# Optimization experiments

Hardware: AMD Instinct MI355X
Metric: run time of the kernel (lower is better)

The kernel has to match this reference:

```python
import jax, jax.numpy as jnp
import numpy as np

N_HEADS = 16


def setup_inputs() -> dict:
    key = jax.random.key(0)
    ks = jax.random.split(key, 5)
    B, S, D = 2, 2048, 1024
    H = N_HEADS
    return {
        "queries": jax.random.normal(ks[0], (B, S, D), dtype=jnp.float32),
        "keys": jax.random.normal(ks[1], (B, S, D), dtype=jnp.float32),
        "values": jax.random.normal(ks[2], (B, S, D), dtype=jnp.float32),
        "bias": jax.random.normal(ks[3], (1, H, S, S), dtype=jnp.float32) * 0.02,
        "w_out": jax.random.normal(ks[4], (D, D), dtype=jnp.float32) * (1.0 / np.sqrt(D)),
    }


def _split_heads(x, n_heads):
    B, S, D = x.shape
    return x.reshape(B, S, n_heads, D // n_heads).transpose(0, 2, 1, 3)  # [B,H,S,hd]


def reference(queries, keys, values, bias, w_out):
    H = N_HEADS
    q = _split_heads(queries, H)
    k = _split_heads(keys, H)
    v = _split_heads(values, H)
    hd = k.shape[-1]
    # NOTE: original adds bias to raw logits, THEN scales by 1/sqrt(dk)
    logits = jnp.einsum("bhqd,bhkd->bhqk", q, k) + bias
    weights = jax.nn.softmax(logits * (1.0 / np.sqrt(hd)), axis=-1)
    attn = jnp.einsum("bhqk,bhkd->bhqd", weights, v)  # [B,H,Sq,hd]
    B, _, Sq, _ = attn.shape
    combined = attn.transpose(0, 2, 1, 3).reshape(B, Sq, H * hd)
    return combined @ w_out
```

## Files before the change

kernel.cpp:

```cpp
#include <hip/hip_runtime.h>

typedef float  f32x4  __attribute__((ext_vector_type(4)));
typedef short  bf16x8 __attribute__((ext_vector_type(8)));
typedef short  s16x4  __attribute__((ext_vector_type(4)));
typedef unsigned int u32x4 __attribute__((ext_vector_type(4)));

#define MFMA_BF16 __builtin_amdgcn_mfma_f32_16x16x32_bf16

__device__ __forceinline__ short f2bf(float f) {
  union { float f; unsigned u; } x; x.f = f;
  unsigned r = x.u + 0x7FFFu + ((x.u >> 16) & 1u);
  return (short)(r >> 16);
}

constexpr int S = 2048, D = 1024, H = 16, HD = 64;
constexpr int NT = S / 64;
constexpr float SCALE = 0.125f;
constexpr float L2E = 1.44269504f;
constexpr float SL = SCALE * L2E;

#define GLDS16(g, l) __builtin_amdgcn_global_load_lds( \
    (const __attribute__((address_space(1))) unsigned*)(g), \
    (__attribute__((address_space(3))) unsigned*)(l), 16, 0, 0)

__global__ __launch_bounds__(256)
void kv_prep(const float* __restrict__ Kg, const float* __restrict__ Vg,
             short* __restrict__ Kb, short* __restrict__ Vb) {
  const int tile = blockIdx.x, h = blockIdx.y, b = blockIdx.z;
  const int t = threadIdx.x, lane = t & 63, w = t >> 6;
  const int lg = lane >> 4, lm = lane & 15;
  __shared__ short kt[64 * 68], vt[64 * 68];
  const float* kp = Kg + ((size_t)(b * S + tile * 64)) * D + h * HD;
  const float* vp = Vg + ((size_t)(b * S + tile * 64)) * D + h * HD;
  #pragma unroll
  for (int i = 0; i < 4; ++i) {
    int idx = i * 256 + t, r = idx >> 4, c4 = (idx & 15) * 4;
    float4 k4 = *(const float4*)(kp + (size_t)r * D + c4);
    s16x4 ks; ks[0]=f2bf(k4.x); ks[1]=f2bf(k4.y); ks[2]=f2bf(k4.z); ks[3]=f2bf(k4.w);
    *(s16x4*)&kt[r * 68 + c4] = ks;
    float4 v4 = *(const float4*)(vp + (size_t)r * D + c4);
    s16x4 vs; vs[0]=f2bf(v4.x); vs[1]=f2bf(v4.y); vs[2]=f2bf(v4.z); vs[3]=f2bf(v4.w);
    *(s16x4*)&vt[r * 68 + c4] = vs;
  }
  __syncthreads();
  const size_t obase = ((size_t)((b * H + h) * NT + tile)) * 4096;
  #pragma unroll
  for (int j = 0; j < 2; ++j) {
    int f = w + j * 4, kk = f >> 2, mf = f & 3;
    int row = mf * 16 + lm, col = kk * 32 + lg * 4;
    s16x4 c0 = *(const s16x4*)&kt[row * 68 + col];
    s16x4 c1 = *(const s16x4*)&kt[row * 68 + col + 16];
    bf16x8 a;
    a[0]=c0[0]; a[1]=c0[1]; a[2]=c0[2]; a[3]=c0[3];
    a[4]=c1[0]; a[5]=c1[1]; a[6]=c1[2]; a[7]=c1[3];
    *(bf16x8*)&Kb[obase + (size_t)(f * 64 + lane) * 8] = a;
  }
  #pragma unroll
  for (int j = 0; j < 2; ++j) {
    int f = w + j * 4, kk = f >> 2, of = f & 3;
    int col = of * 16 + lm;
    bf16x8 a;
    #pragma unroll
    for (int half = 0; half < 2; ++half)
      #pragma unroll
      for (int e = 0; e < 4; ++e)
        a[half * 4 + e] = vt[(kk * 32 + lg * 4 + half * 16 + e) * 68 + col];
    *(bf16x8*)&Vb[obase + (size_t)(f * 64 + lane) * 8] = a;
  }
}

__device__ __forceinline__ void attn_tile(const short* kb, const short* vb,
                                          const f32x4* br, const bf16x8* qf,
                                          int lane, float& M, float& L, f32x4* o) {
  const f32x4 zero4 = {0.f, 0.f, 0.f, 0.f};
  f32x4 sacc[4];
  #pragma unroll
  for (int i = 0; i < 4; ++i) sacc[i] = zero4;
  #pragma unroll
  for (int kk = 0; kk < 2; ++kk)
    #pragma unroll
    for (int mf = 0; mf < 4; ++mf) {
      bf16x8 a = *(const bf16x8*)&kb[(kk * 4 + mf) * 512 + lane * 8];
      sacc[mf] = MFMA_BF16(a, qf[kk], sacc[mf], 0, 0, 0);
    }
  float p[4][4];
  float tmax = -__builtin_inff();
  #pragma unroll
  for (int mf = 0; mf < 4; ++mf)
    #pragma unroll
    for (int j = 0; j < 4; ++j) {
      float tv = (sacc[mf][j] + br[mf][j]) * SL;
      p[mf][j] = tv;
      tmax = fmaxf(tmax, tv);
    }
  tmax = fmaxf(tmax, __shfl_xor(tmax, 16, 64));
  tmax = fmaxf(tmax, __shfl_xor(tmax, 32, 64));
  const float Mn = fmaxf(M, tmax);
  const float alpha = exp2f(M - Mn);
  float psum = 0.f;
  #pragma unroll
  for (int mf = 0; mf < 4; ++mf)
    #pragma unroll
    for (int j = 0; j < 4; ++j) {
      float e = exp2f(p[mf][j] - Mn);
      p[mf][j] = e;
      psum += e;
    }
  psum += __shfl_xor(psum, 16, 64);
  psum += __shfl_xor(psum, 32, 64);
  L = L * alpha + psum;
  M = Mn;
  #pragma unroll
  for (int of = 0; of < 4; ++of) {
    o[of][0] *= alpha; o[of][1] *= alpha; o[of][2] *= alpha; o[of][3] *= alpha;
  }
  bf16x8 pb[2];
  #pragma unroll
  for (int kk = 0; kk < 2; ++kk)
    #pragma unroll
    for (int j = 0; j < 8; ++j)
      pb[kk][j] = f2bf(p[kk * 2 + (j >> 2)][j & 3]);
  #pragma unroll
  for (int kk = 0; kk < 2; ++kk)
    #pragma unroll
    for (int of = 0; of < 4; ++of) {
      bf16x8 a = *(const bf16x8*)&vb[(kk * 4 + of) * 512 + lane * 8];
      o[of] = MFMA_BF16(a, pb[kk], o[of], 0, 0, 0);
    }
}

__global__ __launch_bounds__(256, 4)
void attn_fused(const float* __restrict__ Qg, const float* __restrict__ Bg,
                const short* __restrict__ Kb, const short* __restrict__ Vb,
                short* __restrict__ comb) {
  __shared__ __attribute__((aligned(16))) short smem[16384];
  const int bid = blockIdx.x;
  const int rr = bid >> 4, x = bid & 15;
  const int pairidx = rr * 8 + (x & 7);
  const int b = x >> 3;
  const int h = pairidx >> 5, qt = pairidx & 31;
  const int q0 = qt * 64;
  const int t = threadIdx.x, lane = t & 63, w = t >> 6;
  const int lg = lane >> 4, lm = lane & 15;

  bf16x8 qf[2];
  {
    const float* qp = Qg + ((size_t)(b * S + q0 + w * 16 + lm)) * D + h * HD;
    #pragma unroll
    for (int kk = 0; kk < 2; ++kk)
      #pragma unroll
      for (int j = 0; j < 8; ++j)
        qf[kk][j] = f2bf(qp[kk * 32 + (j >> 2) * 16 + lg * 4 + (j & 3)]);
  }

  const short* Kt = Kb + ((size_t)(b * H + h) * NT) * 4096;
  const short* Vt = Vb + ((size_t)(b * H + h) * NT) * 4096;
  const float* bp = Bg + ((size_t)(h * S + q0 + w * 16 + lm)) * S + lg * 4;

  const f32x4 zero4 = {0.f, 0.f, 0.f, 0.f};
  f32x4 o[4];
  #pragma unroll
  for (int i = 0; i < 4; ++i) o[i] = zero4;
  float M = -__builtin_inff(), L = 0.f;

#define STAGE(tile, kdst, vdst)                                        \
  {                                                                    \
    const short* kg_ = Kt + (size_t)(tile) * 4096;                     \
    const short* vg_ = Vt + (size_t)(tile) * 4096;                     \
    _Pragma("unroll")                                                  \
    for (int r_ = 0; r_ < 2; ++r_) {                                   \
      GLDS16(kg_ + (size_t)((r_ * 4 + w) * 64 + lane) * 8,             \
             (kdst) + (r_ * 4 + w) * 512);                             \
      GLDS16(vg_ + (size_t)((r_ * 4 + w) * 64 + lane) * 8,             \
             (vdst) + (r_ * 4 + w) * 512);                             \
    }                                                                  \
  }

#define BLOAD(dst, tile)                                               \
  {                                                                    \
    const float* bq_ = bp + (tile) * 64;                               \
    dst[0] = *(const f32x4*)(bq_);                                     \
    dst[1] = *(const f32x4*)(bq_ + 16);                                \
    dst[2] = *(const f32x4*)(bq_ + 32);                                \
    dst[3] = *(const f32x4*)(bq_ + 48);                                \
  }

  f32x4 biasA[4], biasB[4];
  STAGE(0, smem, smem + 8192);
  BLOAD(biasA, 0);
  __syncthreads();

  for (int tt = 0; tt < NT; tt += 2) {
    STAGE(tt + 1, smem + 4096, smem + 12288);
    BLOAD(biasB, tt + 1);
    attn_tile(smem, smem + 8192, biasA, qf, lane, M, L, o);
    __syncthreads();
    if (tt + 2 < NT) {
      STAGE(tt + 2, smem, smem + 8192);
      BLOAD(biasA, tt + 2);
    }
    attn_tile(smem + 4096, smem + 12288, biasB, qf, lane, M, L, o);
    __syncthreads();
  }

  const float invL = 1.f / L;
  short* out_lds = smem;
  #pragma unroll
  for (int of = 0; of < 4; ++of)
    #pragma unroll
    for (int j = 0; j < 4; ++j)
      out_lds[(w * 16 + lm) * 72 + of * 16 + lg * 4 + j] = f2bf(o[of][j] * invL);
  __syncthreads();
  #pragma unroll
  for (int it = 0; it < 2; ++it) {
    int idx = it * 256 + t;
    int r = idx >> 3, seg = idx & 7;
    u32x4 u = *(const u32x4*)&out_lds[r * 72 + seg * 8];
    *(u32x4*)&comb[((size_t)(b * S + q0 + r)) * D + h * HD + seg * 8] = u;
  }
#undef STAGE
#undef BLOAD
}

__global__ __launch_bounds__(256)
void wt_kernel(const float* __restrict__ W, short* __restrict__ Wt) {
  __shared__ __attribute__((aligned(16))) short tile[64 * 72];
  const int n0 = blockIdx.x * 64, k0 = blockIdx.y * 64;
  const int t = threadIdx.x;
  #pragma unroll
  for (int i = 0; i < 4; ++i) {
    int idx = i * 256 + t;
    int r  = idx >> 4, c4 = (idx & 15) * 4;
    float4 wv = *(const float4*)(W + (size_t)(k0 + r) * D + n0 + c4);
    tile[(c4 + 0) * 72 + r] = f2bf(wv.x);
    tile[(c4 + 1) * 72 + r] = f2bf(wv.y);
    tile[(c4 + 2) * 72 + r] = f2bf(wv.z);
    tile[(c4 + 3) * 72 + r] = f2bf(wv.w);
  }
  __syncthreads();
  #pragma unroll
  for (int it = 0; it < 2; ++it) {
    int idx = it * 256 + t;
    int r = idx >> 3, seg = idx & 7;
    u32x4 u = *(const u32x4*)&tile[r * 72 + seg * 8];
    *(u32x4*)&Wt[(size_t)(n0 + r) * D + k0 + seg * 8] = u;
  }
}

__global__ __launch_bounds__(256, 2)
void proj_gemm(const short* __restrict__ A, const short* __restrict__ Bt,
               float* __restrict__ C) {
  constexpr int AST = 80;
  __shared__ __attribute__((aligned(16))) short a_lds[128 * AST];
  __shared__ __attribute__((aligned(16))) short b_lds[128 * AST];
  const int m0 = blockIdx.x * 128, n0 = blockIdx.y * 128;
  const int t = threadIdx.x, lane = t & 63, w = t >> 6;
  const int lg = lane >> 4, lm = lane & 15;
  const int wm = w >> 1, wn = w & 1;

  const f32x4 zero4 = {0.f, 0.f, 0.f, 0.f};
  f32x4 acc[4][4];
  #pragma unroll
  for (int i = 0; i < 4; ++i)
    #pragma unroll
    for (int j = 0; j < 4; ++j) acc[i][j] = zero4;

  for (int kt = 0; kt < D; kt += 64) {
    __syncthreads();
    #pragma unroll
    for (int i = 0; i < 4; ++i) {
      int idx = i * 256 + t;
      int r = idx >> 3, seg = idx & 7;
      u32x4 av = *(const u32x4*)&A [(size_t)(m0 + r) * D + kt + seg * 8];
      *(u32x4*)&a_lds[r * AST + seg * 8] = av;
      u32x4 bv = *(const u32x4*)&Bt[(size_t)(n0 + r) * D + kt + seg * 8];
      *(u32x4*)&b_lds[r * AST + seg * 8] = bv;
    }
    __syncthreads();
    #pragma unroll
    for (int kk = 0; kk < 2; ++kk) {
      bf16x8 af[4], bfr[4];
      #pragma unroll
      for (int mf = 0; mf < 4; ++mf) {
        const short* ar = &a_lds[(wm * 64 + mf * 16 + lm) * AST + kk * 32 + lg * 4];
        s16x4 c0 = *(const s16x4*)(ar);
        s16x4 c1 = *(const s16x4*)(ar + 16);
        af[mf][0]=c0[0]; af[mf][1]=c0[1]; af[mf][2]=c0[2]; af[mf][3]=c0[3];
        af[mf][4]=c1[0]; af[mf][5]=c1[1]; af[mf][6]=c1[2]; af[mf][7]=c1[3];
      }
      #pragma unroll
      for (int nf = 0; nf < 4; ++nf) {
        const short* br = &b_lds[(wn * 64 + nf * 16 + lm) * AST + kk * 32 + lg * 4];
        s16x4 c0 = *(const s16x4*)(br);
        s16x4 c1 = *(const s16x4*)(br + 16);
        bfr[nf][0]=c0[0]; bfr[nf][1]=c0[1]; bfr[nf][2]=c0[2]; bfr[nf][3]=c0[3];
        bfr[nf][4]=c1[0]; bfr[nf][5]=c1[1]; bfr[nf][6]=c1[2]; bfr[nf][7]=c1[3];
      }
      #pragma unroll
      for (int mf = 0; mf < 4; ++mf)
        #pragma unroll
        for (int nf = 0; nf < 4; ++nf)
          acc[mf][nf] = MFMA_BF16(af[mf], bfr[nf], acc[mf][nf], 0, 0, 0);
    }
  }
  #pragma unroll
  for (int mf = 0; mf < 4; ++mf)
    #pragma unroll
    for (int j = 0; j < 4; ++j)
      #pragma unroll
      for (int nf = 0; nf < 4; ++nf)
        C[(size_t)(m0 + wm * 64 + mf * 16 + lg * 4 + j) * D +
          n0 + wn * 64 + nf * 16 + lm] = acc[mf][nf][j];
}

extern "C" void kernel_launch(void* const* d_in, const int* in_sizes, int n_in,
                              void* d_out, int out_size, void* d_ws, size_t ws_size,
                              hipStream_t stream) {
  const float* Qg = (const float*)d_in[0];
  const float* Kg = (const float*)d_in[1];
  const float* Vg = (const float*)d_in[2];
  const float* Bg = (const float*)d_in[3];
  const float* Wg = (const float*)d_in[4];
  float* out = (float*)d_out;

  short* comb = (short*)d_ws;
  short* Wt   = comb + (size_t)(2 * S) * D;
  short* Kb   = Wt   + (size_t)D * D;
  short* Vb   = Kb   + (size_t)2 * H * NT * 4096;

  kv_prep<<<dim3(NT, H, 2), 256, 0, stream>>>(Kg, Vg, Kb, Vb);
  wt_kernel<<<dim3(D / 64, D / 64), 256, 0, stream>>>(Wg, Wt);
  attn_fused<<<dim3(1024), 256, 0, stream>>>(Qg, Bg, Kb, Vb, comb);
  proj_gemm<<<dim3((2 * S) / 128, D / 128), 256, 0, stream>>>(comb, Wt, out);
}
```

Baseline: 179.1 us.

## Pipeline projection GEMM with async LDS loads, swizzle, and finer barriers

```diff
diff --git a/kernel.cpp b/kernel.cpp
--- a/kernel.cpp
+++ b/kernel.cpp
@@ -8,9 +8,8 @@
 #define MFMA_BF16 __builtin_amdgcn_mfma_f32_16x16x32_bf16
 
 __device__ __forceinline__ short f2bf(float f) {
-  union { float f; unsigned u; } x; x.f = f;
-  unsigned r = x.u + 0x7FFFu + ((x.u >> 16) & 1u);
-  return (short)(r >> 16);
+  __bf16 h = (__bf16)f;
+  return __builtin_bit_cast(short, h);
 }
 
 constexpr int S = 2048, D = 1024, H = 16, HD = 64;
@@ -22,6 +21,9 @@
 #define GLDS16(g, l) __builtin_amdgcn_global_load_lds( \
     (const __attribute__((address_space(1))) unsigned*)(g), \
     (__attribute__((address_space(3))) unsigned*)(l), 16, 0, 0)
+
+#define WAITV(n) asm volatile("s_waitcnt vmcnt(" #n ")" ::: "memory")
+#define SBAR()   __builtin_amdgcn_s_barrier()
 
 __global__ __launch_bounds__(256)
 void kv_prep(const float* __restrict__ Kg, const float* __restrict__ Vg,
@@ -76,6 +78,7 @@
   f32x4 sacc[4];
   #pragma unroll
   for (int i = 0; i < 4; ++i) sacc[i] = zero4;
+  __builtin_amdgcn_s_setprio(1);
   #pragma unroll
   for (int kk = 0; kk < 2; ++kk)
     #pragma unroll
@@ -83,6 +86,7 @@
       bf16x8 a = *(const bf16x8*)&kb[(kk * 4 + mf) * 512 + lane * 8];
       sacc[mf] = MFMA_BF16(a, qf[kk], sacc[mf], 0, 0, 0);
     }
+  __builtin_amdgcn_s_setprio(0);
   float p[4][4];
   float tmax = -__builtin_inff();
   #pragma unroll
@@ -120,6 +124,7 @@
     #pragma unroll
     for (int j = 0; j < 8; ++j)
       pb[kk][j] = f2bf(p[kk * 2 + (j >> 2)][j & 3]);
+  __builtin_amdgcn_s_setprio(1);
   #pragma unroll
   for (int kk = 0; kk < 2; ++kk)
     #pragma unroll
@@ -127,6 +132,7 @@
       bf16x8 a = *(const bf16x8*)&vb[(kk * 4 + of) * 512 + lane * 8];
       o[of] = MFMA_BF16(a, pb[kk], o[of], 0, 0, 0);
     }
+  __builtin_amdgcn_s_setprio(0);
 }
 
 __global__ __launch_bounds__(256, 4)
@@ -188,22 +194,28 @@
   f32x4 biasA[4], biasB[4];
   STAGE(0, smem, smem + 8192);
   BLOAD(biasA, 0);
-  __syncthreads();
 
   for (int tt = 0; tt < NT; tt += 2) {
+    SBAR();
     STAGE(tt + 1, smem + 4096, smem + 12288);
     BLOAD(biasB, tt + 1);
+    WAITV(8);
+    SBAR();
     attn_tile(smem, smem + 8192, biasA, qf, lane, M, L, o);
-    __syncthreads();
+    SBAR();
     if (tt + 2 < NT) {
       STAGE(tt + 2, smem, smem + 8192);
       BLOAD(biasA, tt + 2);
-    }
+      WAITV(8);
+    } else {
+      WAITV(0);
+    }
+    SBAR();
     attn_tile(smem + 4096, smem + 12288, biasB, qf, lane, M, L, o);
-    __syncthreads();
   }
 
   const float invL = 1.f / L;
+  __syncthreads();
   short* out_lds = smem;
   #pragma unroll
   for (int of = 0; of < 4; ++of)
@@ -247,70 +259,103 @@
   }
 }
 
+__device__ __forceinline__ bf16x8 ld_frag_swz(const short* base, int row, int kk, int lg) {
+  const char* rp = (const char*)base + row * 128 + (lg & 1) * 8;
+  int u0 = kk * 4 + (lg >> 1);
+  int f  = row & 7;
+  s16x4 c0 = *(const s16x4*)(rp + ((u0 ^ f) << 4));
+  s16x4 c1 = *(const s16x4*)(rp + (((u0 + 2) ^ f) << 4));
+  bf16x8 a;
+  a[0]=c0[0]; a[1]=c0[1]; a[2]=c0[2]; a[3]=c0[3];
+  a[4]=c1[0]; a[5]=c1[1]; a[6]=c1[2]; a[7]=c1[3];
+  return a;
+}
+
 __global__ __launch_bounds__(256, 2)
 void proj_gemm(const short* __restrict__ A, const short* __restrict__ Bt,
                float* __restrict__ C) {
-  constexpr int AST = 80;
-  __shared__ __attribute__((aligned(16))) short a_lds[128 * AST];
-  __shared__ __attribute__((aligned(16))) short b_lds[128 * AST];
-  const int m0 = blockIdx.x * 128, n0 = blockIdx.y * 128;
+  __shared__ __attribute__((aligned(16))) short a_lds[2][8192];
+  __shared__ __attribute__((aligned(16))) short b_lds[2][4096];
+  const int m0 = blockIdx.x * 128, n0 = blockIdx.y * 64;
   const int t = threadIdx.x, lane = t & 63, w = t >> 6;
   const int lg = lane >> 4, lm = lane & 15;
-  const int wm = w >> 1, wn = w & 1;
+  const int srow = lane >> 3;
+  const int sunit = (lane & 7) ^ srow;
 
   const f32x4 zero4 = {0.f, 0.f, 0.f, 0.f};
-  f32x4 acc[4][4];
-  #pragma unroll
-  for (int i = 0; i < 4; ++i)
+  f32x4 acc[2][4];
+  #pragma unroll
+  for (int i = 0; i < 2; ++i)
     #pragma unroll
     for (int j = 0; j < 4; ++j) acc[i][j] = zero4;
 
-  for (int kt = 0; kt < D; kt += 64) {
-    __syncthreads();
-    #pragma unroll
-    for (int i = 0; i < 4; ++i) {
-      int idx = i * 256 + t;
-      int r = idx >> 3, seg = idx & 7;
-      u32x4 av = *(const u32x4*)&A [(size_t)(m0 + r) * D + kt + seg * 8];
-      *(u32x4*)&a_lds[r * AST + seg * 8] = av;
-      u32x4 bv = *(const u32x4*)&Bt[(size_t)(n0 + r) * D + kt + seg * 8];
-      *(u32x4*)&b_lds[r * AST + seg * 8] = bv;
-    }
-    __syncthreads();
-    #pragma unroll
-    for (int kk = 0; kk < 2; ++kk) {
-      bf16x8 af[4], bfr[4];
-      #pragma unroll
-      for (int mf = 0; mf < 4; ++mf) {
-        const short* ar = &a_lds[(wm * 64 + mf * 16 + lm) * AST + kk * 32 + lg * 4];
-        s16x4 c0 = *(const s16x4*)(ar);
-        s16x4 c1 = *(const s16x4*)(ar + 16);
-        af[mf][0]=c0[0]; af[mf][1]=c0[1]; af[mf][2]=c0[2]; af[mf][3]=c0[3];
-        af[mf][4]=c1[0]; af[mf][5]=c1[1]; af[mf][6]=c1[2]; af[mf][7]=c1[3];
-      }
-      #pragma unroll
-      for (int nf = 0; nf < 4; ++nf) {
-        const short* br = &b_lds[(wn * 64 + nf * 16 + lm) * AST + kk * 32 + lg * 4];
-        s16x4 c0 = *(const s16x4*)(br);
-        s16x4 c1 = *(const s16x4*)(br + 16);
-        bfr[nf][0]=c0[0]; bfr[nf][1]=c0[1]; bfr[nf][2]=c0[2]; bfr[nf][3]=c0[3];
-        bfr[nf][4]=c1[0]; bfr[nf][5]=c1[1]; bfr[nf][6]=c1[2]; bfr[nf][7]=c1[3];
-      }
-      #pragma unroll
-      for (int mf = 0; mf < 4; ++mf)
-        #pragma unroll
-        for (int nf = 0; nf < 4; ++nf)
-          acc[mf][nf] = MFMA_BF16(af[mf], bfr[nf], acc[mf][nf], 0, 0, 0);
-    }
-  }
-  #pragma unroll
-  for (int mf = 0; mf < 4; ++mf)
+#define PSTAGE(ks, ab, bb)                                                  \
+  {                                                                         \
+    const short* ag_ = A  + (size_t)m0 * D + (ks) * 64;                     \
+    const short* bg_ = Bt + (size_t)n0 * D + (ks) * 64;                     \
+    _Pragma("unroll")                                                       \
+    for (int i_ = 0; i_ < 4; ++i_) {                                        \
+      int j_ = w * 4 + i_;                                                  \
+      GLDS16(ag_ + (size_t)(j_ * 8 + srow) * D + sunit * 8, (ab) + j_ * 512); \
+    }                                                                       \
+    _Pragma("unroll")                                                       \
+    for (int i_ = 0; i_ < 2; ++i_) {                                        \
+      int j_ = w * 2 + i_;                                                  \
+      GLDS16(bg_ + (size_t)(j_ * 8 + srow) * D + sunit * 8, (bb) + j_ * 512); \
+    }                                                                       \
+  }
+
+#define PCOMPUTE(ab, bb)                                                    \
+  {                                                                         \
+    _Pragma("unroll")                                                       \
+    for (int kk = 0; kk < 2; ++kk) {                                        \
+      bf16x8 af0 = ld_frag_swz(ab, w * 32 + lm, kk, lg);                    \
+      bf16x8 af1 = ld_frag_swz(ab, w * 32 + 16 + lm, kk, lg);               \
+      bf16x8 bf0 = ld_frag_swz(bb, lm, kk, lg);                             \
+      bf16x8 bf1 = ld_frag_swz(bb, 16 + lm, kk, lg);                        \
+      bf16x8 bf2 = ld_frag_swz(bb, 32 + lm, kk, lg);                        \
+      bf16x8 bf3 = ld_frag_swz(bb, 48 + lm, kk, lg);                        \
+      __builtin_amdgcn_s_setprio(1);                                        \
+      acc[0][0] = MFMA_BF16(af0, bf0, acc[0][0], 0, 0, 0);                  \
+      acc[0][1] = MFMA_BF16(af0, bf1, acc[0][1], 0, 0, 0);                  \
+      acc[0][2] = MFMA_BF16(af0, bf2, acc[0][2], 0, 0, 0);                  \
+      acc[0][3] = MFMA_BF16(af0, bf3, acc[0][3], 0, 0, 0);                  \
+      acc[1][0] = MFMA_BF16(af1, bf0, acc[1][0], 0, 0, 0);                  \
+      acc[1][1] = MFMA_BF16(af1, bf1, acc[1][1], 0, 0, 0);                  \
+      acc[1][2] = MFMA_BF16(af1, bf2, acc[1][2], 0, 0, 0);                  \
+      acc[1][3] = MFMA_BF16(af1, bf3, acc[1][3], 0, 0, 0);                  \
+      __builtin_amdgcn_s_setprio(0);                                        \
+    }                                                                       \
+  }
+
+  PSTAGE(0, a_lds[0], b_lds[0]);
+  for (int ks = 0; ks < 16; ks += 2) {
+    SBAR();
+    PSTAGE(ks + 1, a_lds[1], b_lds[1]);
+    WAITV(6);
+    SBAR();
+    PCOMPUTE(a_lds[0], b_lds[0]);
+    SBAR();
+    if (ks + 2 < 16) {
+      PSTAGE(ks + 2, a_lds[0], b_lds[0]);
+      WAITV(6);
+    } else {
+      WAITV(0);
+    }
+    SBAR();
+    PCOMPUTE(a_lds[1], b_lds[1]);
+  }
+
+  #pragma unroll
+  for (int mf = 0; mf < 2; ++mf)
     #pragma unroll
     for (int j = 0; j < 4; ++j)
       #pragma unroll
       for (int nf = 0; nf < 4; ++nf)
-        C[(size_t)(m0 + wm * 64 + mf * 16 + lg * 4 + j) * D +
-          n0 + wn * 64 + nf * 16 + lm] = acc[mf][nf][j];
+        C[(size_t)(m0 + w * 32 + mf * 16 + lg * 4 + j) * D +
+          n0 + nf * 16 + lm] = acc[mf][nf][j];
+#undef PSTAGE
+#undef PCOMPUTE
 }
 
 extern "C" void kernel_launch(void* const* d_in, const int* in_sizes, int n_in,
@@ -331,5 +376,5 @@
   kv_prep<<<dim3(NT, H, 2), 256, 0, stream>>>(Kg, Vg, Kb, Vb);
   wt_kernel<<<dim3(D / 64, D / 64), 256, 0, stream>>>(Wg, Wt);
   attn_fused<<<dim3(1024), 256, 0, stream>>>(Qg, Bg, Kb, Vb, comb);
-  proj_gemm<<<dim3((2 * S) / 128, D / 128), 256, 0, stream>>>(comb, Wt, out);
-}
+  proj_gemm<<<dim3(32, 16), 256, 0, stream>>>(comb, Wt, out);
+}
```

After: 150.6 us. 15.9% less time.
